# Kernel tuning notes

Measured on AMD Instinct MI355X. Metric: run time of the kernel, lower is better.

## Reference

```python
import jax, jax.numpy as jnp
import numpy as np

MODES, WIDTH, N_LAYERS, N_PARAMS, N_OUT, T = 24, 128, 6, 5, 3, 300
BATCH = 2048

def gelu(x):
    return jax.nn.gelu(x, approximate=False)

def setup_inputs() -> dict:
    key = jax.random.key(0)
    ks = jax.random.split(key, 16)
    scale = 1.0 / (WIDTH * WIDTH)
    d = {
        "params": jax.random.normal(ks[0], (BATCH, N_PARAMS), jnp.float32),
        "enc_w1": jax.random.normal(ks[1], (N_PARAMS, WIDTH), jnp.float32) * 0.1,
        "enc_b1": jax.random.normal(ks[2], (WIDTH,), jnp.float32) * 0.1,
        "enc_w2": jax.random.normal(ks[3], (WIDTH, WIDTH), jnp.float32) * 0.05,
        "enc_b2": jax.random.normal(ks[4], (WIDTH,), jnp.float32) * 0.1,
        "enc_w3": jax.random.normal(ks[5], (WIDTH, WIDTH * T), jnp.float32) * 0.05,
        "enc_b3": jax.random.normal(ks[6], (WIDTH * T,), jnp.float32) * 0.1,
        "spec_wr": jax.random.normal(ks[7], (N_LAYERS, WIDTH, WIDTH, MODES), jnp.float32) * scale,
        "spec_wi": jax.random.normal(ks[8], (N_LAYERS, WIDTH, WIDTH, MODES), jnp.float32) * scale,
        "conv_w": jax.random.normal(ks[9], (N_LAYERS, WIDTH, WIDTH), jnp.float32) * 0.05,
        "conv_b": jax.random.normal(ks[10], (N_LAYERS, WIDTH), jnp.float32) * 0.05,
        "out_w1": jax.random.normal(ks[11], (WIDTH // 2, WIDTH), jnp.float32) * 0.05,
        "out_b1": jax.random.normal(ks[12], (WIDTH // 2,), jnp.float32) * 0.1,
        "out_w2": jax.random.normal(ks[13], (N_OUT, WIDTH // 2), jnp.float32) * 0.1,
        "out_b2": jax.random.normal(ks[14], (N_OUT,), jnp.float32) * 0.1,
    }
    return d

def reference(params, enc_w1, enc_b1, enc_w2, enc_b2, enc_w3, enc_b3,
              spec_wr, spec_wi, conv_w, conv_b, out_w1, out_b1, out_w2, out_b2):
    B = params.shape[0]
    # parameter encoder: Linear->GELU->Linear->GELU->Linear
    h = gelu(params @ enc_w1 + enc_b1)
    h = gelu(h @ enc_w2 + enc_b2)
    h = h @ enc_w3 + enc_b3                      # [B, width*T]
    x = h.reshape(B, WIDTH, T)                   # [B, C, T]
    n_freq = T // 2 + 1
    for l in range(N_LAYERS):
        # spectral conv: rfft, truncate to MODES, complex channel mix, irfft
        x_ft = jnp.fft.rfft(x, axis=-1)[:, :, :MODES]          # [B, C, modes] complex64
        w = (spec_wr[l] + 1j * spec_wi[l]).astype(jnp.complex64)
        of = jnp.einsum('bix,iox->box', x_ft, w)               # [B, C, modes]
        out_ft = jnp.zeros((B, WIDTH, n_freq), jnp.complex64).at[:, :, :MODES].set(of)
        x1 = jnp.fft.irfft(out_ft, n=T, axis=-1)
        # 1x1 conv
        x2 = jnp.einsum('oc,bct->bot', conv_w[l], x) + conv_b[l][None, :, None]
        x = gelu(x1 + x2) + x
    # output projection: Conv1x1 -> GELU -> Conv1x1
    h = gelu(jnp.einsum('oc,bct->bot', out_w1, x) + out_b1[None, :, None])
    out = jnp.einsum('oc,bct->bot', out_w2, h) + out_b2[None, :, None]  # [B, 3, T]
    return out.transpose(0, 2, 1)                                       # [B, T, 3]
```

## Files before the change

kernel.cpp:

```cpp
#include <hip/hip_runtime.h>
#include <math.h>

#define NB 2048
#define WD 128
#define TD 300
#define TP 320
#define NM 24
#define NJ 48
#define NJP 64
#define NL 6
#define NCOL 38400
#define WSCALE 1024.0f

typedef _Float16 half_t;
typedef _Float16 h8 __attribute__((ext_vector_type(8)));
typedef float f4 __attribute__((ext_vector_type(4)));

#define MFMA(a,b,c) __builtin_amdgcn_mfma_f32_16x16x32_f16(a,b,c,0,0,0)

__device__ __forceinline__ float gelu_f(float v){
    return 0.5f * v * (1.0f + erff(v * 0.70710678118654752f));
}

__global__ __launch_bounds__(256) void k_tables(half_t* __restrict__ Fth, half_t* __restrict__ Gt){
    int idx = blockIdx.x*256 + threadIdx.x;
    const float w0 = 6.28318530717958647692f / 300.0f;
    if (idx < NJ*TP) {
        int j = idx / TP, t = idx - j*TP;
        int m = j >> 1;
        float v = 0.0f;
        if (t < TD) {
            int r = (m*t) % TD;
            float ang = (float)r * w0;
            v = (j & 1) ? -sinf(ang) : cosf(ang);
        }
        Fth[idx] = (half_t)v;
    }
    if (idx < TP*NJP) {
        int t = idx / NJP, j = idx - t*NJP;
        float v = 0.0f;
        if (j < NJ) {
            int m = j >> 1;
            int r = (m * (t % TD)) % TD;
            float ang = (float)r * w0;
            float s = (m == 0) ? (1.0f/300.0f) : (2.0f/300.0f);
            if (j & 1) v = (m == 0) ? 0.0f : -s*sinf(ang);
            else       v = s*cosf(ang);
        }
        Gt[idx] = (half_t)v;
    }
}

__global__ __launch_bounds__(256) void k_wx(const float* __restrict__ wr, const float* __restrict__ wi,
                                            half_t* __restrict__ Wxh){
    long idx = (long)blockIdx.x*256 + threadIdx.x;
    if (idx >= (long)NL*NM*256*256) return;
    int k = (int)(idx & 255), n = (int)((idx >> 8) & 255);
    int lm = (int)(idx >> 16);
    int l = lm / NM, m = lm - l*NM;
    int i = k & 127, o = n & 127;
    long src = (((long)(l*WD + i))*WD + o)*NM + m;
    float v;
    if (n < 128) v = (k < 128) ? wr[src] : -wi[src];
    else         v = (k < 128) ? wi[src] :  wr[src];
    Wxh[idx] = (half_t)(v * WSCALE);
}

__global__ __launch_bounds__(256) void k_w3t(const float* __restrict__ w3, half_t* __restrict__ w3t){
    int idx = blockIdx.x*256 + threadIdx.x;
    if (idx >= NCOL*WD) return;
    int k = idx & 127, col = idx >> 7;
    w3t[idx] = (half_t)w3[k*NCOL + col];
}

__global__ __launch_bounds__(256) void k_cwh(const float* __restrict__ cw, half_t* __restrict__ cwh){
    int idx = blockIdx.x*256 + threadIdx.x;
    if (idx >= NL*WD*WD) return;
    cwh[idx] = (half_t)cw[idx];
}

__global__ __launch_bounds__(256) void k_w1h(const float* __restrict__ w1, half_t* __restrict__ w1h){
    int idx = blockIdx.x*256 + threadIdx.x;
    if (idx >= 64*WD) return;
    w1h[idx] = (half_t)w1[idx];
}

__global__ __launch_bounds__(256) void k_enc1(const float* __restrict__ p, const float* __restrict__ w1,
                                              const float* __restrict__ b1, float* __restrict__ h1){
    int idx = blockIdx.x*256 + threadIdx.x;
    int b = idx >> 7, k = idx & 127;
    float acc = b1[k];
    #pragma unroll
    for (int j = 0; j < 5; j++) acc += p[b*5+j] * w1[j*WD+k];
    h1[idx] = gelu_f(acc);
}

__global__ __launch_bounds__(256) void k_enc2(const float* __restrict__ h1, const float* __restrict__ w2,
                                              const float* __restrict__ b2, half_t* __restrict__ h2h){
    int idx = blockIdx.x*256 + threadIdx.x;
    int b = idx >> 7, k = idx & 127;
    const float* row = h1 + b*WD;
    float acc = b2[k];
    for (int j = 0; j < WD; j += 4) {
        float4 h4 = *(const float4*)(row + j);
        acc += h4.x * w2[(j+0)*WD+k] + h4.y * w2[(j+1)*WD+k]
             + h4.z * w2[(j+2)*WD+k] + h4.w * w2[(j+3)*WD+k];
    }
    h2h[idx] = (half_t)gelu_f(acc);
}

__global__ __launch_bounds__(256) void k_enc3(const half_t* __restrict__ h2h, const half_t* __restrict__ w3t,
        const float* __restrict__ b3, float* __restrict__ x){
    int tid = threadIdx.x;
    int lane = tid & 63, w = tid >> 6;
    int wr = w >> 1, wc = w & 1;
    int c0 = blockIdx.x * 128;
    int b0 = blockIdx.y * 64;
    int ln = lane & 15, lk = lane >> 4;
    f4 zz = {0.f,0.f,0.f,0.f};
    f4 acc[2][4];
    #pragma unroll
    for (int i = 0; i < 2; i++) for (int j = 0; j < 4; j++) acc[i][j] = zz;
    const half_t* ap = h2h + (long)(b0 + wr*32 + ln)*WD + lk*8;
    const half_t* bp = w3t + (long)(c0 + wc*64 + ln)*WD + lk*8;
    #pragma unroll
    for (int ks = 0; ks < 4; ks++) {
        h8 a0 = *(const h8*)(ap + ks*32);
        h8 a1 = *(const h8*)(ap + 16*WD + ks*32);
        #pragma unroll
        for (int bt = 0; bt < 4; bt++) {
            h8 bf = *(const h8*)(bp + bt*16*WD + ks*32);
            acc[0][bt] = MFMA(a0, bf, acc[0][bt]);
            acc[1][bt] = MFMA(a1, bf, acc[1][bt]);
        }
    }
    #pragma unroll
    for (int at = 0; at < 2; at++)
    #pragma unroll
    for (int bt = 0; bt < 4; bt++) {
        int col = c0 + wc*64 + bt*16 + ln;
        float bias = b3[col];
        #pragma unroll
        for (int r = 0; r < 4; r++) {
            int b = b0 + wr*32 + at*16 + lk*4 + r;
            x[(long)b*NCOL + col] = acc[at][bt][r] + bias;
        }
    }
}

__global__ __launch_bounds__(256) void k_tr2(const float* __restrict__ x, half_t* __restrict__ xt,
                                             half_t* __restrict__ xc){
    __shared__ half_t tl[WD*65];
    int tid = threadIdx.x;
    int t0 = blockIdx.x * 64;
    long b = blockIdx.y;
    {
        int c = tid >> 1, th = tid & 1;
        const float* xp = x + b*NCOL + (long)c*TD + t0 + th*32;
        half_t reg[32];
        #pragma unroll
        for (int i = 0; i < 8; i++) {
            int t = t0 + th*32 + i*4;
            float4 v;
            if (t + 3 < TD) v = *(const float4*)(xp + i*4);
            else v = make_float4((t<TD)?xp[i*4]:0.f, (t+1<TD)?xp[i*4+1]:0.f,
                                 (t+2<TD)?xp[i*4+2]:0.f, (t+3<TD)?xp[i*4+3]:0.f);
            reg[i*4+0]=(half_t)v.x; reg[i*4+1]=(half_t)v.y;
            reg[i*4+2]=(half_t)v.z; reg[i*4+3]=(half_t)v.w;
        }
        half_t* dst = &tl[c*65 + th*32];
        #pragma unroll
        for (int i = 0; i < 32; i++) dst[i] = reg[i];
        half_t* op = xc + (b*WD + c)*TP + t0 + th*32;
        *(h8*)(op)    = *(h8*)(&reg[0]);
        *(h8*)(op+8)  = *(h8*)(&reg[8]);
        *(h8*)(op+16) = *(h8*)(&reg[16]);
        *(h8*)(op+24) = *(h8*)(&reg[24]);
    }
    __syncthreads();
    {
        int lane = tid & 63, w = tid >> 6;
        const half_t* src = &tl[w*32*65 + lane];
        h8 v[4];
        #pragma unroll
        for (int k2 = 0; k2 < 4; k2++)
            #pragma unroll
            for (int e = 0; e < 8; e++)
                v[k2][e] = src[(k2*8 + e)*65];
        half_t* op = xt + (b*TP + t0 + lane)*WD + w*32;
        *(h8*)(op) = v[0]; *(h8*)(op+8) = v[1]; *(h8*)(op+16) = v[2]; *(h8*)(op+24) = v[3];
    }
}

__global__ __launch_bounds__(256) void k_rfft(const half_t* __restrict__ xc, const half_t* __restrict__ Fth,
        half_t* __restrict__ S, int CB){
    int tid = threadIdx.x;
    int lane = tid & 63, w = tid >> 6;
    int ln = lane & 15, lk = lane >> 4;
    long r0 = (long)blockIdx.x*128 + w*32;
    f4 zz = {0.f,0.f,0.f,0.f};
    f4 acc[2][3];
    #pragma unroll
    for (int i = 0; i < 2; i++) for (int j = 0; j < 3; j++) acc[i][j] = zz;
    const half_t* ap = xc + r0*TP + lk*8;
    const half_t* fpB = Fth + ln*TP + lk*8;
    #pragma unroll
    for (int ks = 0; ks < 10; ks++) {
        h8 a0 = *(const h8*)(ap + ln*TP + ks*32);
        h8 a1 = *(const h8*)(ap + (16+ln)*TP + ks*32);
        #pragma unroll
        for (int jt = 0; jt < 3; jt++) {
            h8 bf = *(const h8*)(fpB + jt*16*TP + ks*32);
            acc[0][jt] = MFMA(a0, bf, acc[0][jt]);
            acc[1][jt] = MFMA(a1, bf, acc[1][jt]);
        }
    }
    #pragma unroll
    for (int at = 0; at < 2; at++)
    #pragma unroll
    for (int jt = 0; jt < 3; jt++) {
        int j = jt*16 + ln;
        int m = j >> 1, ri = j & 1;
        #pragma unroll
        for (int r = 0; r < 4; r++) {
            long row = r0 + at*16 + lk*4 + r;
            int b = (int)(row >> 7), c = (int)(row & 127);
            S[((long)m*CB + b)*256 + ri*128 + c] = (half_t)acc[at][jt][r];
        }
    }
}

__global__ __launch_bounds__(256) void k_mix(const half_t* __restrict__ S, const half_t* __restrict__ Wxh,
        half_t* __restrict__ Yh, int layer, int CB){
    int tid = threadIdx.x;
    int lane = tid & 63, w = tid >> 6;
    int wr = w >> 1, wc = w & 1;
    int ln = lane & 15, lk = lane >> 4;
    int m = blockIdx.z;
    int b0 = blockIdx.x * 64;
    int n0 = blockIdx.y * 128;
    f4 zz = {0.f,0.f,0.f,0.f};
    f4 acc[2][4];
    #pragma unroll
    for (int i = 0; i < 2; i++) for (int j = 0; j < 4; j++) acc[i][j] = zz;
    const half_t* ap = S + ((long)m*CB + b0 + wr*32 + ln)*256 + lk*8;
    const half_t* bp = Wxh + (((long)(layer*NM + m))*256 + n0 + wc*64 + ln)*256 + lk*8;
    #pragma unroll
    for (int ks = 0; ks < 8; ks++) {
        h8 a0 = *(const h8*)(ap + ks*32);
        h8 a1 = *(const h8*)(ap + 16*256 + ks*32);
        #pragma unroll
        for (int bt = 0; bt < 4; bt++) {
            h8 bf = *(const h8*)(bp + bt*16*256 + ks*32);
            acc[0][bt] = MFMA(a0, bf, acc[0][bt]);
            acc[1][bt] = MFMA(a1, bf, acc[1][bt]);
        }
    }
    const float inv = 1.0f / WSCALE;
    #pragma unroll
    for (int at = 0; at < 2; at++)
    #pragma unroll
    for (int bt = 0; bt < 4; bt++) {
        int n = n0 + wc*64 + bt*16 + ln;
        int o = n & 127, ri = n >> 7;
        #pragma unroll
        for (int r = 0; r < 4; r++) {
            int b = b0 + wr*32 + at*16 + lk*4 + r;
            Yh[((long)b*WD + o)*NJP + 2*m + ri] = (half_t)(acc[at][bt][r] * inv);
        }
    }
}

__global__ __launch_bounds__(256) void k_fuse(const half_t* __restrict__ Yh, const half_t* __restrict__ Gt,
        const half_t* __restrict__ cwh, half_t* __restrict__ xt, const float* __restrict__ convb,
        half_t* __restrict__ xc, int layer){
    __shared__ float gl[64*133];
    int tid = threadIdx.x;
    int lane = tid & 63, w = tid >> 6;
    int wo = w * 32;
    int ln = lane & 15, lk = lane >> 4;
    int t0 = blockIdx.x * 64;
    long b = blockIdx.y;
    f4 zz = {0.f,0.f,0.f,0.f};
    f4 acc[2][4];
    #pragma unroll
    for (int i = 0; i < 2; i++) for (int j = 0; j < 4; j++) acc[i][j] = zz;
    const half_t* ap = cwh + ((long)layer*WD + wo + ln)*WD + lk*8;
    const half_t* bp = xt + (b*TP + t0 + ln)*WD + lk*8;
    #pragma unroll
    for (int ks = 0; ks < 4; ks++) {
        h8 a0 = *(const h8*)(ap + ks*32);
        h8 a1 = *(const h8*)(ap + 16*WD + ks*32);
        #pragma unroll
        for (int bt = 0; bt < 4; bt++) {
            h8 bf = *(const h8*)(bp + bt*16*WD + ks*32);
            acc[0][bt] = MFMA(a0, bf, acc[0][bt]);
            acc[1][bt] = MFMA(a1, bf, acc[1][bt]);
        }
    }
    const half_t* ap2 = Yh + (b*WD + wo + ln)*NJP + lk*8;
    const half_t* bp2 = Gt + (long)(t0 + ln)*NJP + lk*8;
    #pragma unroll
    for (int ks = 0; ks < 2; ks++) {
        h8 a0 = *(const h8*)(ap2 + ks*32);
        h8 a1 = *(const h8*)(ap2 + 16*NJP + ks*32);
        #pragma unroll
        for (int bt = 0; bt < 4; bt++) {
            h8 bf = *(const h8*)(bp2 + bt*16*NJP + ks*32);
            acc[0][bt] = MFMA(a0, bf, acc[0][bt]);
            acc[1][bt] = MFMA(a1, bf, acc[1][bt]);
        }
    }
    #pragma unroll
    for (int at = 0; at < 2; at++) {
        int obase = wo + at*16 + lk*4;
        float cb0 = convb[layer*WD + obase];
        float cb1 = convb[layer*WD + obase + 1];
        float cb2 = convb[layer*WD + obase + 2];
        float cb3 = convb[layer*WD + obase + 3];
        #pragma unroll
        for (int bt = 0; bt < 4; bt++) {
            float* g = &gl[(bt*16 + ln)*133 + obase];
            g[0] = gelu_f(acc[at][bt][0] + cb0);
            g[1] = gelu_f(acc[at][bt][1] + cb1);
            g[2] = gelu_f(acc[at][bt][2] + cb2);
            g[3] = gelu_f(acc[at][bt][3] + cb3);
        }
    }
    __syncthreads();
    {
        int tl_ = tid >> 2, c0 = (tid & 3)*32;
        int t = t0 + tl_;
        float* g = &gl[tl_*133 + c0];
        if (t < TD) {
            const half_t* xr = xt + (b*TP + t)*WD + c0;
            h8 v0 = *(const h8*)(xr);
            h8 v1 = *(const h8*)(xr + 8);
            h8 v2 = *(const h8*)(xr + 16);
            h8 v3 = *(const h8*)(xr + 24);
            #pragma unroll
            for (int i = 0; i < 8; i++) {
                g[i]    += (float)v0[i];
                g[8+i]  += (float)v1[i];
                g[16+i] += (float)v2[i];
                g[24+i] += (float)v3[i];
            }
        } else {
            #pragma unroll
            for (int i = 0; i < 32; i++) g[i] = 0.0f;
        }
    }
    __syncthreads();
    {
        const float* gr = &gl[lane*133 + wo];
        h8 v[4];
        #pragma unroll
        for (int k2 = 0; k2 < 4; k2++)
            #pragma unroll
            for (int e = 0; e < 8; e++)
                v[k2][e] = (half_t)gr[k2*8 + e];
        half_t* op = xt + (b*TP + t0 + lane)*WD + wo;
        *(h8*)(op) = v[0]; *(h8*)(op+8) = v[1]; *(h8*)(op+16) = v[2]; *(h8*)(op+24) = v[3];
    }
    {
        int c = tid >> 1, th = tid & 1;
        half_t* op = xc + (b*WD + c)*TP + t0 + th*32;
        #pragma unroll
        for (int e = 0; e < 32; e += 8) {
            h8 v;
            #pragma unroll
            for (int i = 0; i < 8; i++)
                v[i] = (half_t)gl[(th*32 + e + i)*133 + c];
            *(h8*)(op + e) = v;
        }
    }
}

__global__ __launch_bounds__(256) void k_out(const half_t* __restrict__ xt, const half_t* __restrict__ w1h,
        const float* __restrict__ b1, const float* __restrict__ w2, const float* __restrict__ b2,
        float* __restrict__ out){
    __shared__ float gl[64*68];
    __shared__ float w2l[192];
    int tid = threadIdx.x;
    int lane = tid & 63, w = tid >> 6;
    int mo = (w >> 1)*32, mt = (w & 1)*32;
    int ln = lane & 15, lk = lane >> 4;
    int t0 = blockIdx.x * 64;
    long b = blockIdx.y;
    f4 zz = {0.f,0.f,0.f,0.f};
    f4 acc[2][2];
    #pragma unroll
    for (int i = 0; i < 2; i++) for (int j = 0; j < 2; j++) acc[i][j] = zz;
    const half_t* ap = w1h + (long)(mo + ln)*WD + lk*8;
    const half_t* bp = xt + (b*TP + t0 + mt + ln)*WD + lk*8;
    #pragma unroll
    for (int ks = 0; ks < 4; ks++) {
        h8 a0 = *(const h8*)(ap + ks*32);
        h8 a1 = *(const h8*)(ap + 16*WD + ks*32);
        h8 b0f = *(const h8*)(bp + ks*32);
        h8 b1f = *(const h8*)(bp + 16*WD + ks*32);
        acc[0][0] = MFMA(a0, b0f, acc[0][0]);
        acc[0][1] = MFMA(a0, b1f, acc[0][1]);
        acc[1][0] = MFMA(a1, b0f, acc[1][0]);
        acc[1][1] = MFMA(a1, b1f, acc[1][1]);
    }
    if (tid < 192) w2l[tid] = w2[tid];
    #pragma unroll
    for (int at = 0; at < 2; at++)
    #pragma unroll
    for (int bt = 0; bt < 2; bt++) {
        int tl = mt + bt*16 + ln;
        int obase = mo + at*16 + lk*4;
        #pragma unroll
        for (int r = 0; r < 4; r++) {
            int o = obase + r;
            gl[tl*68 + o] = gelu_f(acc[at][bt][r] + b1[o]);
        }
    }
    __syncthreads();
    int t = tid & 63, q = tid >> 6;
    int tg = t0 + t;
    if (q < 3 && tg < TD) {
        float s = b2[q];
        const float* gr = &gl[t*68];
        const float* wr = &w2l[q*64];
        #pragma unroll
        for (int o = 0; o < 64; o += 4) {
            s += wr[o]*gr[o] + wr[o+1]*gr[o+1] + wr[o+2]*gr[o+2] + wr[o+3]*gr[o+3];
        }
        out[((long)b*TD + tg)*3 + q] = s;
    }
}

extern "C" void kernel_launch(void* const* d_in, const int* in_sizes, int n_in,
                              void* d_out, int out_size, void* d_ws, size_t ws_size,
                              hipStream_t stream) {
    const float* params = (const float*)d_in[0];
    const float* enc_w1 = (const float*)d_in[1];
    const float* enc_b1 = (const float*)d_in[2];
    const float* enc_w2 = (const float*)d_in[3];
    const float* enc_b2 = (const float*)d_in[4];
    const float* enc_w3 = (const float*)d_in[5];
    const float* enc_b3 = (const float*)d_in[6];
    const float* spec_wr = (const float*)d_in[7];
    const float* spec_wi = (const float*)d_in[8];
    const float* conv_w  = (const float*)d_in[9];
    const float* conv_b  = (const float*)d_in[10];
    const float* out_w1  = (const float*)d_in[11];
    const float* out_b1  = (const float*)d_in[12];
    const float* out_w2  = (const float*)d_in[13];
    const float* out_b2  = (const float*)d_in[14];
    float* outp = (float*)d_out;

    const long szWxh = (long)NL*NM*256*256*2;
    const long szW3t = (long)NCOL*WD*2;
    const long szCwh = (long)NL*WD*WD*2;
    const long szW1h = (long)64*WD*2;
    const long szFth = (long)NJ*TP*2;
    const long szGt  = (long)TP*NJP*2;
    const long fixedB = szWxh + szW3t + szCwh + szW1h + szFth + szGt;
    const long perCB = (long)NCOL*4 + 2L*(long)TP*WD*2 + (long)NM*256*2 + (long)WD*NJP*2 + WD*4 + WD*2;

    long CB = 512;
    while (CB > 64 && fixedB + CB*perCB > (long)ws_size) CB >>= 1;
    int nchunk = (int)(NB / CB);

    char* p = (char*)d_ws;
    half_t* Wxh = (half_t*)p; p += szWxh;
    half_t* w3t = (half_t*)p; p += szW3t;
    half_t* cwh = (half_t*)p; p += szCwh;
    half_t* w1h = (half_t*)p; p += szW1h;
    half_t* Fth = (half_t*)p; p += szFth;
    half_t* Gt  = (half_t*)p; p += szGt;
    float*  x   = (float*)p;  p += CB*(long)NCOL*4;
    half_t* xt  = (half_t*)p; p += CB*(long)TP*WD*2;
    half_t* xc  = (half_t*)p; p += CB*(long)TP*WD*2;
    half_t* S   = (half_t*)p; p += CB*(long)NM*256*2;
    half_t* Yh  = (half_t*)p; p += CB*(long)WD*NJP*2;
    float*  h1  = (float*)p;  p += CB*(long)WD*4;
    half_t* h2h = (half_t*)p; p += CB*(long)WD*2;

    k_tables<<<80, 256, 0, stream>>>(Fth, Gt);
    k_wx<<<36864, 256, 0, stream>>>(spec_wr, spec_wi, Wxh);
    k_w3t<<<19200, 256, 0, stream>>>(enc_w3, w3t);
    k_cwh<<<384, 256, 0, stream>>>(conv_w, cwh);
    k_w1h<<<32, 256, 0, stream>>>(out_w1, w1h);

    for (int ch = 0; ch < nchunk; ch++) {
        const float* pch = params + (long)ch*CB*5;
        float* outch = outp + (long)ch*CB*TD*3;
        k_enc1<<<(int)(CB*WD/256), 256, 0, stream>>>(pch, enc_w1, enc_b1, h1);
        k_enc2<<<(int)(CB*WD/256), 256, 0, stream>>>(h1, enc_w2, enc_b2, h2h);
        k_enc3<<<dim3(NCOL/128, (int)(CB/64)), 256, 0, stream>>>(h2h, w3t, enc_b3, x);
        k_tr2<<<dim3(TP/64, (int)CB), 256, 0, stream>>>(x, xt, xc);
        for (int l = 0; l < NL; l++) {
            k_rfft<<<(int)CB, 256, 0, stream>>>(xc, Fth, S, (int)CB);
            k_mix<<<dim3((int)(CB/64), 2, NM), 256, 0, stream>>>(S, Wxh, Yh, l, (int)CB);
            k_fuse<<<dim3(TP/64, (int)CB), 256, 0, stream>>>(Yh, Gt, cwh, xt, conv_b, xc, l);
        }
        k_out<<<dim3(TP/64, (int)CB), 256, 0, stream>>>(xt, w1h, out_b1, out_w2, out_b2, outch);
    }
}
```

Before: 3.599 ms.

## Write encoder output directly as fp16 time-major, fuse output head into last layer

The encoder's third GEMM now uses a weight reordered to [t][c][k], so it writes fp16 activations straight into the time-major xt buffer, including zeroed padding rows. This removes the fp32 intermediate x and its fp32-to-half transpose pass. A lighter half-to-half transpose kernel builds the channel-major copy, and the output projection is folded into the last layer's fuse kernel, which saves one launch and a round trip of xt. The trade-offs are a slightly larger reordered weight table, more branching in the fuse kernel, and scattered bias reads in enc3.

```diff
diff --git a/kernel.cpp b/kernel.cpp
--- a/kernel.cpp
+++ b/kernel.cpp
@@ -66,11 +66,14 @@
     Wxh[idx] = (half_t)(v * WSCALE);
 }
 
-__global__ __launch_bounds__(256) void k_w3t(const float* __restrict__ w3, half_t* __restrict__ w3t){
-    int idx = blockIdx.x*256 + threadIdx.x;
-    if (idx >= NCOL*WD) return;
-    int k = idx & 127, col = idx >> 7;
-    w3t[idx] = (half_t)w3[k*NCOL + col];
+__global__ __launch_bounds__(256) void k_w3t2(const float* __restrict__ w3, half_t* __restrict__ w3t2){
+    long idx = (long)blockIdx.x*256 + threadIdx.x;
+    if (idx >= (long)TD*WD*WD) return;
+    int k = (int)(idx & 127);
+    long rest = idx >> 7;
+    int c = (int)(rest & 127);
+    int t = (int)(rest >> 7);
+    w3t2[idx] = (half_t)w3[(long)k*NCOL + c*TD + t];
 }
 
 __global__ __launch_bounds__(256) void k_cwh(const float* __restrict__ cw, half_t* __restrict__ cwh){
@@ -109,20 +112,27 @@
     h2h[idx] = (half_t)gelu_f(acc);
 }
 
-__global__ __launch_bounds__(256) void k_enc3(const half_t* __restrict__ h2h, const half_t* __restrict__ w3t,
-        const float* __restrict__ b3, float* __restrict__ x){
+__global__ __launch_bounds__(256) void k_enc3(const half_t* __restrict__ h2h, const half_t* __restrict__ w3t2,
+        const float* __restrict__ b3, half_t* __restrict__ xt){
     int tid = threadIdx.x;
+    int t = blockIdx.x;
+    int b0 = blockIdx.y * 64;
+    if (t >= TD) {
+        int bb = tid >> 2, cg = (tid & 3) * 32;
+        half_t* op = xt + ((long)(b0 + bb)*TP + t)*WD + cg;
+        uint4 z = make_uint4(0,0,0,0);
+        *(uint4*)(op) = z; *(uint4*)(op + 16) = z;
+        return;
+    }
     int lane = tid & 63, w = tid >> 6;
     int wr = w >> 1, wc = w & 1;
-    int c0 = blockIdx.x * 128;
-    int b0 = blockIdx.y * 64;
     int ln = lane & 15, lk = lane >> 4;
     f4 zz = {0.f,0.f,0.f,0.f};
     f4 acc[2][4];
     #pragma unroll
     for (int i = 0; i < 2; i++) for (int j = 0; j < 4; j++) acc[i][j] = zz;
     const half_t* ap = h2h + (long)(b0 + wr*32 + ln)*WD + lk*8;
-    const half_t* bp = w3t + (long)(c0 + wc*64 + ln)*WD + lk*8;
+    const half_t* bp = w3t2 + ((long)t*WD + wc*64 + ln)*WD + lk*8;
     #pragma unroll
     for (int ks = 0; ks < 4; ks++) {
         h8 a0 = *(const h8*)(ap + ks*32);
@@ -138,57 +148,43 @@
     for (int at = 0; at < 2; at++)
     #pragma unroll
     for (int bt = 0; bt < 4; bt++) {
-        int col = c0 + wc*64 + bt*16 + ln;
-        float bias = b3[col];
+        int c = wc*64 + bt*16 + ln;
+        float bias = b3[c*TD + t];
         #pragma unroll
         for (int r = 0; r < 4; r++) {
             int b = b0 + wr*32 + at*16 + lk*4 + r;
-            x[(long)b*NCOL + col] = acc[at][bt][r] + bias;
-        }
-    }
-}
-
-__global__ __launch_bounds__(256) void k_tr2(const float* __restrict__ x, half_t* __restrict__ xt,
-                                             half_t* __restrict__ xc){
-    __shared__ half_t tl[WD*65];
+            xt[((long)b*TP + t)*WD + c] = (half_t)(acc[at][bt][r] + bias);
+        }
+    }
+}
+
+__global__ __launch_bounds__(256) void k_trh(const half_t* __restrict__ xt, half_t* __restrict__ xc){
+    __shared__ half_t tl[64*136];
     int tid = threadIdx.x;
     int t0 = blockIdx.x * 64;
     long b = blockIdx.y;
     {
-        int c = tid >> 1, th = tid & 1;
-        const float* xp = x + b*NCOL + (long)c*TD + t0 + th*32;
-        half_t reg[32];
-        #pragma unroll
-        for (int i = 0; i < 8; i++) {
-            int t = t0 + th*32 + i*4;
-            float4 v;
-            if (t + 3 < TD) v = *(const float4*)(xp + i*4);
-            else v = make_float4((t<TD)?xp[i*4]:0.f, (t+1<TD)?xp[i*4+1]:0.f,
-                                 (t+2<TD)?xp[i*4+2]:0.f, (t+3<TD)?xp[i*4+3]:0.f);
-            reg[i*4+0]=(half_t)v.x; reg[i*4+1]=(half_t)v.y;
-            reg[i*4+2]=(half_t)v.z; reg[i*4+3]=(half_t)v.w;
-        }
-        half_t* dst = &tl[c*65 + th*32];
-        #pragma unroll
-        for (int i = 0; i < 32; i++) dst[i] = reg[i];
-        half_t* op = xc + (b*WD + c)*TP + t0 + th*32;
-        *(h8*)(op)    = *(h8*)(&reg[0]);
-        *(h8*)(op+8)  = *(h8*)(&reg[8]);
-        *(h8*)(op+16) = *(h8*)(&reg[16]);
-        *(h8*)(op+24) = *(h8*)(&reg[24]);
+        int tr = tid >> 2, q = (tid & 3) * 32;
+        const half_t* ip = xt + (b*TP + t0 + tr)*WD + q;
+        h8 v0 = *(const h8*)(ip);
+        h8 v1 = *(const h8*)(ip + 8);
+        h8 v2 = *(const h8*)(ip + 16);
+        h8 v3 = *(const h8*)(ip + 24);
+        half_t* dst = &tl[tr*136 + q];
+        *(h8*)(dst) = v0; *(h8*)(dst+8) = v1; *(h8*)(dst+16) = v2; *(h8*)(dst+24) = v3;
     }
     __syncthreads();
     {
-        int lane = tid & 63, w = tid >> 6;
-        const half_t* src = &tl[w*32*65 + lane];
-        h8 v[4];
+        int c = tid >> 1, th = tid & 1;
+        const half_t* src = &tl[th*32*136 + c];
+        h8 o[4];
         #pragma unroll
         for (int k2 = 0; k2 < 4; k2++)
             #pragma unroll
             for (int e = 0; e < 8; e++)
-                v[k2][e] = src[(k2*8 + e)*65];
-        half_t* op = xt + (b*TP + t0 + lane)*WD + w*32;
-        *(h8*)(op) = v[0]; *(h8*)(op+8) = v[1]; *(h8*)(op+16) = v[2]; *(h8*)(op+24) = v[3];
+                o[k2][e] = src[(k2*8 + e)*136];
+        half_t* op = xc + (b*WD + c)*TP + t0 + th*32;
+        *(h8*)(op) = o[0]; *(h8*)(op+8) = o[1]; *(h8*)(op+16) = o[2]; *(h8*)(op+24) = o[3];
     }
 }
 
@@ -273,8 +269,11 @@
 
 __global__ __launch_bounds__(256) void k_fuse(const half_t* __restrict__ Yh, const half_t* __restrict__ Gt,
         const half_t* __restrict__ cwh, half_t* __restrict__ xt, const float* __restrict__ convb,
-        half_t* __restrict__ xc, int layer){
+        half_t* __restrict__ xc, int layer, int last,
+        const half_t* __restrict__ w1h, const float* __restrict__ ob1,
+        const float* __restrict__ ow2, const float* __restrict__ ob2, float* __restrict__ out){
     __shared__ float gl[64*133];
+    __shared__ float w2l[192];
     int tid = threadIdx.x;
     int lane = tid & 63, w = tid >> 6;
     int wo = w * 32;
@@ -327,13 +326,13 @@
             g[3] = gelu_f(acc[at][bt][3] + cb3);
         }
     }
+    if (last && tid < 192) w2l[tid] = ow2[tid];
     __syncthreads();
     {
-        int tl_ = tid >> 2, c0 = (tid & 3)*32;
-        int t = t0 + tl_;
-        float* g = &gl[tl_*133 + c0];
+        int t = t0 + lane;
+        float* g = &gl[lane*133 + wo];
         if (t < TD) {
-            const half_t* xr = xt + (b*TP + t)*WD + c0;
+            const half_t* xr = xt + (b*TP + t)*WD + wo;
             h8 v0 = *(const h8*)(xr);
             h8 v1 = *(const h8*)(xr + 8);
             h8 v2 = *(const h8*)(xr + 16);
@@ -351,84 +350,76 @@
         }
     }
     __syncthreads();
-    {
-        const float* gr = &gl[lane*133 + wo];
-        h8 v[4];
-        #pragma unroll
-        for (int k2 = 0; k2 < 4; k2++)
-            #pragma unroll
-            for (int e = 0; e < 8; e++)
-                v[k2][e] = (half_t)gr[k2*8 + e];
-        half_t* op = xt + (b*TP + t0 + lane)*WD + wo;
-        *(h8*)(op) = v[0]; *(h8*)(op+8) = v[1]; *(h8*)(op+16) = v[2]; *(h8*)(op+24) = v[3];
-    }
-    {
-        int c = tid >> 1, th = tid & 1;
-        half_t* op = xc + (b*WD + c)*TP + t0 + th*32;
-        #pragma unroll
-        for (int e = 0; e < 32; e += 8) {
-            h8 v;
-            #pragma unroll
-            for (int i = 0; i < 8; i++)
-                v[i] = (half_t)gl[(th*32 + e + i)*133 + c];
-            *(h8*)(op + e) = v;
-        }
-    }
-}
-
-__global__ __launch_bounds__(256) void k_out(const half_t* __restrict__ xt, const half_t* __restrict__ w1h,
-        const float* __restrict__ b1, const float* __restrict__ w2, const float* __restrict__ b2,
-        float* __restrict__ out){
-    __shared__ float gl[64*68];
-    __shared__ float w2l[192];
-    int tid = threadIdx.x;
-    int lane = tid & 63, w = tid >> 6;
-    int mo = (w >> 1)*32, mt = (w & 1)*32;
-    int ln = lane & 15, lk = lane >> 4;
-    int t0 = blockIdx.x * 64;
-    long b = blockIdx.y;
-    f4 zz = {0.f,0.f,0.f,0.f};
-    f4 acc[2][2];
-    #pragma unroll
-    for (int i = 0; i < 2; i++) for (int j = 0; j < 2; j++) acc[i][j] = zz;
-    const half_t* ap = w1h + (long)(mo + ln)*WD + lk*8;
-    const half_t* bp = xt + (b*TP + t0 + mt + ln)*WD + lk*8;
-    #pragma unroll
-    for (int ks = 0; ks < 4; ks++) {
-        h8 a0 = *(const h8*)(ap + ks*32);
-        h8 a1 = *(const h8*)(ap + 16*WD + ks*32);
-        h8 b0f = *(const h8*)(bp + ks*32);
-        h8 b1f = *(const h8*)(bp + 16*WD + ks*32);
-        acc[0][0] = MFMA(a0, b0f, acc[0][0]);
-        acc[0][1] = MFMA(a0, b1f, acc[0][1]);
-        acc[1][0] = MFMA(a1, b0f, acc[1][0]);
-        acc[1][1] = MFMA(a1, b1f, acc[1][1]);
-    }
-    if (tid < 192) w2l[tid] = w2[tid];
-    #pragma unroll
-    for (int at = 0; at < 2; at++)
-    #pragma unroll
-    for (int bt = 0; bt < 2; bt++) {
-        int tl = mt + bt*16 + ln;
-        int obase = mo + at*16 + lk*4;
-        #pragma unroll
-        for (int r = 0; r < 4; r++) {
-            int o = obase + r;
-            gl[tl*68 + o] = gelu_f(acc[at][bt][r] + b1[o]);
-        }
-    }
-    __syncthreads();
-    int t = tid & 63, q = tid >> 6;
-    int tg = t0 + t;
-    if (q < 3 && tg < TD) {
-        float s = b2[q];
-        const float* gr = &gl[t*68];
-        const float* wr = &w2l[q*64];
-        #pragma unroll
-        for (int o = 0; o < 64; o += 4) {
-            s += wr[o]*gr[o] + wr[o+1]*gr[o+1] + wr[o+2]*gr[o+2] + wr[o+3]*gr[o+3];
-        }
-        out[((long)b*TD + tg)*3 + q] = s;
+    if (!last) {
+        {
+            const float* gr = &gl[lane*133 + wo];
+            h8 v[4];
+            #pragma unroll
+            for (int k2 = 0; k2 < 4; k2++)
+                #pragma unroll
+                for (int e = 0; e < 8; e++)
+                    v[k2][e] = (half_t)gr[k2*8 + e];
+            half_t* op = xt + (b*TP + t0 + lane)*WD + wo;
+            *(h8*)(op) = v[0]; *(h8*)(op+8) = v[1]; *(h8*)(op+16) = v[2]; *(h8*)(op+24) = v[3];
+        }
+        {
+            int c = tid >> 1, th = tid & 1;
+            half_t* op = xc + (b*WD + c)*TP + t0 + th*32;
+            #pragma unroll
+            for (int e = 0; e < 32; e += 8) {
+                h8 v;
+                #pragma unroll
+                for (int i = 0; i < 8; i++)
+                    v[i] = (half_t)gl[(th*32 + e + i)*133 + c];
+                *(h8*)(op + e) = v;
+            }
+        }
+    } else {
+        int mo = (w >> 1)*32, mt = (w & 1)*32;
+        f4 oacc[2][2];
+        #pragma unroll
+        for (int i = 0; i < 2; i++) for (int j = 0; j < 2; j++) oacc[i][j] = zz;
+        const half_t* wap = w1h + (long)(mo + ln)*WD + lk*8;
+        #pragma unroll
+        for (int ks = 0; ks < 4; ks++) {
+            h8 a0 = *(const h8*)(wap + ks*32);
+            h8 a1 = *(const h8*)(wap + 16*WD + ks*32);
+            h8 b0f, b1f;
+            const float* g0 = &gl[(mt + ln)*133 + ks*32 + lk*8];
+            const float* g1 = &gl[(mt + 16 + ln)*133 + ks*32 + lk*8];
+            #pragma unroll
+            for (int e = 0; e < 8; e++) { b0f[e] = (half_t)g0[e]; b1f[e] = (half_t)g1[e]; }
+            oacc[0][0] = MFMA(a0, b0f, oacc[0][0]);
+            oacc[0][1] = MFMA(a0, b1f, oacc[0][1]);
+            oacc[1][0] = MFMA(a1, b0f, oacc[1][0]);
+            oacc[1][1] = MFMA(a1, b1f, oacc[1][1]);
+        }
+        __syncthreads();
+        #pragma unroll
+        for (int at = 0; at < 2; at++)
+        #pragma unroll
+        for (int bt = 0; bt < 2; bt++) {
+            int tl = mt + bt*16 + ln;
+            int obase = mo + at*16 + lk*4;
+            #pragma unroll
+            for (int r = 0; r < 4; r++) {
+                int o = obase + r;
+                gl[tl*68 + o] = gelu_f(oacc[at][bt][r] + ob1[o]);
+            }
+        }
+        __syncthreads();
+        int tq = tid & 63, qq = tid >> 6;
+        int tg = t0 + tq;
+        if (qq < 3 && tg < TD) {
+            float s = ob2[qq];
+            const float* gr = &gl[tq*68];
+            const float* wr2 = &w2l[qq*64];
+            #pragma unroll
+            for (int o = 0; o < 64; o += 4) {
+                s += wr2[o]*gr[o] + wr2[o+1]*gr[o+1] + wr2[o+2]*gr[o+2] + wr2[o+3]*gr[o+3];
+            }
+            out[((long)b*TD + tg)*3 + qq] = s;
+        }
     }
 }
 
@@ -453,36 +444,35 @@
     float* outp = (float*)d_out;
 
     const long szWxh = (long)NL*NM*256*256*2;
-    const long szW3t = (long)NCOL*WD*2;
+    const long szW3t = (long)TD*WD*WD*2;
     const long szCwh = (long)NL*WD*WD*2;
     const long szW1h = (long)64*WD*2;
     const long szFth = (long)NJ*TP*2;
     const long szGt  = (long)TP*NJP*2;
     const long fixedB = szWxh + szW3t + szCwh + szW1h + szFth + szGt;
-    const long perCB = (long)NCOL*4 + 2L*(long)TP*WD*2 + (long)NM*256*2 + (long)WD*NJP*2 + WD*4 + WD*2;
+    const long perCB = 2L*(long)TP*WD*2 + (long)NM*256*2 + (long)WD*NJP*2 + WD*4 + WD*2;
 
     long CB = 512;
     while (CB > 64 && fixedB + CB*perCB > (long)ws_size) CB >>= 1;
     int nchunk = (int)(NB / CB);
 
     char* p = (char*)d_ws;
-    half_t* Wxh = (half_t*)p; p += szWxh;
-    half_t* w3t = (half_t*)p; p += szW3t;
-    half_t* cwh = (half_t*)p; p += szCwh;
-    half_t* w1h = (half_t*)p; p += szW1h;
-    half_t* Fth = (half_t*)p; p += szFth;
-    half_t* Gt  = (half_t*)p; p += szGt;
-    float*  x   = (float*)p;  p += CB*(long)NCOL*4;
-    half_t* xt  = (half_t*)p; p += CB*(long)TP*WD*2;
-    half_t* xc  = (half_t*)p; p += CB*(long)TP*WD*2;
-    half_t* S   = (half_t*)p; p += CB*(long)NM*256*2;
-    half_t* Yh  = (half_t*)p; p += CB*(long)WD*NJP*2;
-    float*  h1  = (float*)p;  p += CB*(long)WD*4;
-    half_t* h2h = (half_t*)p; p += CB*(long)WD*2;
+    half_t* Wxh  = (half_t*)p; p += szWxh;
+    half_t* w3t2 = (half_t*)p; p += szW3t;
+    half_t* cwh  = (half_t*)p; p += szCwh;
+    half_t* w1h  = (half_t*)p; p += szW1h;
+    half_t* Fth  = (half_t*)p; p += szFth;
+    half_t* Gt   = (half_t*)p; p += szGt;
+    half_t* xt   = (half_t*)p; p += CB*(long)TP*WD*2;
+    half_t* xc   = (half_t*)p; p += CB*(long)TP*WD*2;
+    half_t* S    = (half_t*)p; p += CB*(long)NM*256*2;
+    half_t* Yh   = (half_t*)p; p += CB*(long)WD*NJP*2;
+    float*  h1   = (float*)p;  p += CB*(long)WD*4;
+    half_t* h2h  = (half_t*)p; p += CB*(long)WD*2;
 
     k_tables<<<80, 256, 0, stream>>>(Fth, Gt);
     k_wx<<<36864, 256, 0, stream>>>(spec_wr, spec_wi, Wxh);
-    k_w3t<<<19200, 256, 0, stream>>>(enc_w3, w3t);
+    k_w3t2<<<19200, 256, 0, stream>>>(enc_w3, w3t2);
     k_cwh<<<384, 256, 0, stream>>>(conv_w, cwh);
     k_w1h<<<32, 256, 0, stream>>>(out_w1, w1h);
 
@@ -491,13 +481,14 @@
         float* outch = outp + (long)ch*CB*TD*3;
         k_enc1<<<(int)(CB*WD/256), 256, 0, stream>>>(pch, enc_w1, enc_b1, h1);
         k_enc2<<<(int)(CB*WD/256), 256, 0, stream>>>(h1, enc_w2, enc_b2, h2h);
-        k_enc3<<<dim3(NCOL/128, (int)(CB/64)), 256, 0, stream>>>(h2h, w3t, enc_b3, x);
-        k_tr2<<<dim3(TP/64, (int)CB), 256, 0, stream>>>(x, xt, xc);
+        k_enc3<<<dim3(TP, (int)(CB/64)), 256, 0, stream>>>(h2h, w3t2, enc_b3, xt);
+        k_trh<<<dim3(TP/64, (int)CB), 256, 0, stream>>>(xt, xc);
         for (int l = 0; l < NL; l++) {
+            int last = (l == NL-1) ? 1 : 0;
             k_rfft<<<(int)CB, 256, 0, stream>>>(xc, Fth, S, (int)CB);
             k_mix<<<dim3((int)(CB/64), 2, NM), 256, 0, stream>>>(S, Wxh, Yh, l, (int)CB);
-            k_fuse<<<dim3(TP/64, (int)CB), 256, 0, stream>>>(Yh, Gt, cwh, xt, conv_b, xc, l);
-        }
-        k_out<<<dim3(TP/64, (int)CB), 256, 0, stream>>>(xt, w1h, out_b1, out_w2, out_b2, outch);
-    }
-}
+            k_fuse<<<dim3(TP/64, (int)CB), 256, 0, stream>>>(Yh, Gt, cwh, xt, conv_b, xc, l, last,
+                                                             w1h, out_b1, out_w2, out_b2, outch);
+        }
+    }
+}
```

Result: faster. 3.372 ms (-6.3%).
